# Kernel tuning notes

Measured on AMD Instinct MI355X. Metric: run time of the kernel, lower is better.

Reference implementation:

```python
import jax, jax.numpy as jnp
import numpy as np

E, B, DX, DC, DH, DO = 16, 4096, 128, 64, 1024, 128
DIN = DX + DC

def setup_inputs() -> dict:
    key = jax.random.key(0)
    ks = jax.random.split(key, 6)
    s1 = 1.0 / np.sqrt(DIN)
    s2 = 1.0 / np.sqrt(DH)
    return {
        "x": jax.random.normal(ks[0], (E, B, DX), dtype=jnp.float32),
        "cond": jax.random.normal(ks[1], (E, B, DC), dtype=jnp.float32),
        # stacked per-expert params, mirroring param_stacks ([E, ...])
        "W1": jax.random.uniform(ks[2], (E, DH, DIN), minval=-s1, maxval=s1, dtype=jnp.float32),
        "b1": jax.random.uniform(ks[3], (E, DH), minval=-s1, maxval=s1, dtype=jnp.float32),
        "W2": jax.random.uniform(ks[4], (E, DO, DH), minval=-s2, maxval=s2, dtype=jnp.float32),
        "b2": jax.random.uniform(ks[5], (E, DO), minval=-s2, maxval=s2, dtype=jnp.float32),
    }

def reference(x, cond, W1, b1, W2, b2):
    # vmap over experts == grouped GEMM with per-expert weight tiles
    xc = jnp.concatenate([x, cond], axis=-1)          # [E, B, DIN]
    h = jnp.einsum('ebi,ehi->ebh', xc, W1) + b1[:, None, :]  # [E, B, DH]
    h = jax.nn.relu(h)
    y = jnp.einsum('ebh,eoh->ebo', h, W2) + b2[:, None, :]   # [E, B, DO]
    return y
```

## Files before the change

### kernel.cpp

```cpp
#include <hip/hip_runtime.h>
#include <hip/hip_bf16.h>

#define E_   16
#define B_   4096
#define DX_  128
#define DC_  64
#define DIN_ 192
#define DH_  1024
#define DO_  128

#define BM 256
#define KC 64
#define NCHUNK 16
#define NT 1024

#define W1B_OFF 0
#define W1B_STR 12288
#define W2B_OFF 24576
#define W2B_STR 8192
#define HB_OFF  40960
#define HB_STR  16384

#define NW1U2 (E_ * DH_ * DIN_ / 4)
#define NW2U2 (E_ * DO_ * DH_ / 4)
#define WS_BYTES ((size_t)(NW1U2 + NW2U2) * 8)

typedef __attribute__((ext_vector_type(4))) float f32x4;
typedef __attribute__((ext_vector_type(8))) short bf16x8;

__device__ __forceinline__ unsigned f2bf_u(float f) {
    union { float f; unsigned u; } v; v.f = f;
    return (v.u + 0x7fffu + ((v.u >> 16) & 1u)) >> 16;
}
__device__ __forceinline__ uint2 pack4(float4 v) {
    uint2 r;
    r.x = f2bf_u(v.x) | (f2bf_u(v.y) << 16);
    r.y = f2bf_u(v.z) | (f2bf_u(v.w) << 16);
    return r;
}
__device__ __forceinline__ int swz(int r, int S, int cb) {
    return r * S + ((cb ^ ((r & 7) << 4)) >> 1);
}
__device__ __forceinline__ bf16x8 load8cvt(const float* p) {
    float4 a = *(const float4*)p;
    float4 b = *(const float4*)(p + 4);
    bf16x8 r;
    r[0] = (short)f2bf_u(a.x); r[1] = (short)f2bf_u(a.y);
    r[2] = (short)f2bf_u(a.z); r[3] = (short)f2bf_u(a.w);
    r[4] = (short)f2bf_u(b.x); r[5] = (short)f2bf_u(b.y);
    r[6] = (short)f2bf_u(b.z); r[7] = (short)f2bf_u(b.w);
    return r;
}
__device__ __forceinline__ void gld_lds16(const void* g, void* l) {
    __builtin_amdgcn_global_load_lds(
        (const __attribute__((address_space(1))) unsigned int*)g,
        (__attribute__((address_space(3))) unsigned int*)l, 16, 0, 0);
}

__global__ __launch_bounds__(256)
void convert_w(const float4* __restrict__ W1, const float4* __restrict__ W2,
               uint2* __restrict__ ws) {
    const int ntot = NW1U2 + NW2U2;
    for (int i = blockIdx.x * 256 + threadIdx.x; i < ntot; i += gridDim.x * 256) {
        if (i < NW1U2) {
            float4 v = W1[i];
            int e  = i / (DH_ * 48);
            int rr = i - e * (DH_ * 48);
            int hr = rr / 48, cu = rr - hr * 48;
            int ch = hr >> 6, r = hr & 63;
            int S  = swz(r, DIN_, cu * 8);
            ws[(size_t)(e * 16 + ch) * 3072 + (S >> 2)] = pack4(v);
        } else {
            ws[i] = pack4(W2[i - NW1U2]);
        }
    }
}

template <bool WS>
__global__ __launch_bounds__(NT, 4)
void moe_fused_kernel(const float* __restrict__ x, const float* __restrict__ cond,
                      const float* __restrict__ W1, const float* __restrict__ b1,
                      const float* __restrict__ W2, const float* __restrict__ b2,
                      const uint2* __restrict__ wsw, float* __restrict__ out) {
    __shared__ short LDSU[73728];

    const int bid = blockIdx.x;
    const int xcd = bid & 7;
    const int s   = bid >> 3;
    const int e   = 2 * xcd + (s & 1);
    const int row0 = (s >> 1) * BM;

    const int tid  = threadIdx.x;
    const int w    = tid >> 6;
    const int lane = tid & 63;
    const int lr   = lane & 15;
    const int lg   = lane >> 4;
    const int wo   = w & 1;
    const int wm   = w >> 1;

    const char*  ws1b = (const char*)wsw;
    const uint2* ws2  = wsw + NW1U2 + (size_t)e * (DO_ * DH_ / 4);
    const float4* g1f = (const float4*)(W1 + (size_t)e * DH_ * DIN_);
    const float*  g2f = W2 + (size_t)e * DO_ * DH_;

    bf16x8 xcreg[6];
    {
        const float* xrow = x    + (size_t)(e * B_ + row0 + w * 16 + lr) * DX_;
        const float* crow = cond + (size_t)(e * B_ + row0 + w * 16 + lr) * DC_;
#pragma unroll
        for (int kk = 0; kk < 4; ++kk) xcreg[kk] = load8cvt(xrow + kk * 32 + lg * 8);
#pragma unroll
        for (int kk = 4; kk < 6; ++kk) xcreg[kk] = load8cvt(crow + (kk - 4) * 32 + lg * 8);
    }

    uint2  r2[2]; float4 r2f[2]; float4 r1f[3];
    if constexpr (WS) {
        for (int q = w; q < 24; q += 16)
            gld_lds16(ws1b + (size_t)(e * 16 + 0) * 24576 + q * 1024 + lane * 16,
                      (char*)&LDSU[W1B_OFF] + q * 1024);
#pragma unroll
        for (int i = 0; i < 2; ++i) {
            int g = tid + NT * i, r = g >> 4, cc = g & 15;
            r2[i] = ws2[r * 256 + cc];
        }
    } else {
#pragma unroll
        for (int i = 0; i < 3; ++i) r1f[i] = g1f[tid + NT * i];
#pragma unroll
        for (int i = 0; i < 3; ++i) {
            int g = tid + NT * i, r = g / 48, cu = g - r * 48;
            *(uint2*)&LDSU[W1B_OFF + swz(r, DIN_, cu * 8)] = pack4(r1f[i]);
        }
#pragma unroll
        for (int i = 0; i < 3; ++i) r1f[i] = g1f[3072 + tid + NT * i];
#pragma unroll
        for (int i = 0; i < 2; ++i) {
            int g = tid + NT * i, r = g >> 4, cc = g & 15;
            r2f[i] = *(const float4*)(g2f + (size_t)r * DH_ + cc * 4);
        }
    }
    __syncthreads();

    f32x4 acc2[4][2] = {};

    for (int c = 0; c < NCHUNK; ++c) {
        const int pc = c & 1, pp = pc ^ 1;

#pragma unroll
        for (int i = 0; i < 2; ++i) {
            int g = tid + NT * i, r = g >> 4, cc = g & 15;
            uint2 pv; if constexpr (WS) pv = r2[i]; else pv = pack4(r2f[i]);
            *(uint2*)&LDSU[W2B_OFF + pc * W2B_STR + swz(r, KC, cc * 8)] = pv;
        }
        if (c + 1 < NCHUNK) {
            if constexpr (WS) {
                for (int q = w; q < 24; q += 16)
                    gld_lds16(ws1b + (size_t)(e * 16 + c + 1) * 24576 + q * 1024 + lane * 16,
                              (char*)&LDSU[W1B_OFF + pp * W1B_STR] + q * 1024);
            } else {
#pragma unroll
                for (int i = 0; i < 3; ++i) {
                    int g = tid + NT * i, r = g / 48, cu = g - r * 48;
                    *(uint2*)&LDSU[W1B_OFF + pp * W1B_STR + swz(r, DIN_, cu * 8)] = pack4(r1f[i]);
                }
                if (c + 2 < NCHUNK) {
#pragma unroll
                    for (int i = 0; i < 3; ++i) r1f[i] = g1f[(c + 2) * 3072 + tid + NT * i];
                }
            }
        }
        if (c + 1 < NCHUNK) {
            if constexpr (WS) {
#pragma unroll
                for (int i = 0; i < 2; ++i) {
                    int g = tid + NT * i, r = g >> 4, cc = g & 15;
                    r2[i] = ws2[r * 256 + (c + 1) * 16 + cc];
                }
            } else {
#pragma unroll
                for (int i = 0; i < 2; ++i) {
                    int g = tid + NT * i, r = g >> 4, cc = g & 15;
                    r2f[i] = *(const float4*)(g2f + (size_t)r * DH_ + (c + 1) * KC + cc * 4);
                }
            }
        }

        if (c > 0) {
#pragma unroll
            for (int kk = 0; kk < 2; ++kk) {
                bf16x8 aW2[4], bH[2];
#pragma unroll
                for (int of = 0; of < 4; ++of)
                    aW2[of] = *(const bf16x8*)&LDSU[W2B_OFF + pp * W2B_STR + swz(wo * 64 + of * 16 + lr, KC, kk * 64 + lg * 16)];
#pragma unroll
                for (int nf = 0; nf < 2; ++nf)
                    bH[nf] = *(const bf16x8*)&LDSU[HB_OFF + pp * HB_STR + swz(wm * 32 + nf * 16 + lr, KC, kk * 64 + lg * 16)];
#pragma unroll
                for (int of = 0; of < 4; ++of)
#pragma unroll
                    for (int nf = 0; nf < 2; ++nf)
                        acc2[of][nf] = __builtin_amdgcn_mfma_f32_16x16x32_bf16(aW2[of], bH[nf], acc2[of][nf], 0, 0, 0);
            }
        }

        f32x4 acc1[4] = {};
#pragma unroll
        for (int kk = 0; kk < 6; ++kk) {
            bf16x8 aW[4];
#pragma unroll
            for (int hf = 0; hf < 4; ++hf)
                aW[hf] = *(const bf16x8*)&LDSU[W1B_OFF + pc * W1B_STR + swz(hf * 16 + lr, DIN_, kk * 64 + lg * 16)];
#pragma unroll
            for (int hf = 0; hf < 4; ++hf)
                acc1[hf] = __builtin_amdgcn_mfma_f32_16x16x32_bf16(aW[hf], xcreg[kk], acc1[hf], 0, 0, 0);
        }
#pragma unroll
        for (int hf = 0; hf < 4; ++hf) {
            float4 b1f = *(const float4*)&b1[e * DH_ + c * KC + hf * 16 + lg * 4];
            float v0 = fmaxf(acc1[hf][0] + b1f.x, 0.f);
            float v1 = fmaxf(acc1[hf][1] + b1f.y, 0.f);
            float v2 = fmaxf(acc1[hf][2] + b1f.z, 0.f);
            float v3 = fmaxf(acc1[hf][3] + b1f.w, 0.f);
            uint2 hv;
            hv.x = f2bf_u(v0) | (f2bf_u(v1) << 16);
            hv.y = f2bf_u(v2) | (f2bf_u(v3) << 16);
            int m = w * 16 + lr;
            *(uint2*)&LDSU[HB_OFF + pc * HB_STR + swz(m, KC, hf * 32 + lg * 8)] = hv;
        }

        __syncthreads();
    }

#pragma unroll
    for (int kk = 0; kk < 2; ++kk) {
        bf16x8 aW2[4], bH[2];
#pragma unroll
        for (int of = 0; of < 4; ++of)
            aW2[of] = *(const bf16x8*)&LDSU[W2B_OFF + W2B_STR + swz(wo * 64 + of * 16 + lr, KC, kk * 64 + lg * 16)];
#pragma unroll
        for (int nf = 0; nf < 2; ++nf)
            bH[nf] = *(const bf16x8*)&LDSU[HB_OFF + HB_STR + swz(wm * 32 + nf * 16 + lr, KC, kk * 64 + lg * 16)];
#pragma unroll
        for (int of = 0; of < 4; ++of)
#pragma unroll
            for (int nf = 0; nf < 2; ++nf)
                acc2[of][nf] = __builtin_amdgcn_mfma_f32_16x16x32_bf16(aW2[of], bH[nf], acc2[of][nf], 0, 0, 0);
    }

#pragma unroll
    for (int of = 0; of < 4; ++of) {
        float4 b2f = *(const float4*)&b2[e * DO_ + wo * 64 + of * 16 + lg * 4];
#pragma unroll
        for (int nf = 0; nf < 2; ++nf) {
            int m = wm * 32 + nf * 16 + lr;
            float4 val;
            val.x = acc2[of][nf][0] + b2f.x;
            val.y = acc2[of][nf][1] + b2f.y;
            val.z = acc2[of][nf][2] + b2f.z;
            val.w = acc2[of][nf][3] + b2f.w;
            *(float4*)&out[(size_t)(e * B_ + row0 + m) * DO_ + wo * 64 + of * 16 + lg * 4] = val;
        }
    }
}

extern "C" void kernel_launch(void* const* d_in, const int* in_sizes, int n_in,
                              void* d_out, int out_size, void* d_ws, size_t ws_size,
                              hipStream_t stream) {
    const float* x    = (const float*)d_in[0];
    const float* cond = (const float*)d_in[1];
    const float* W1   = (const float*)d_in[2];
    const float* b1   = (const float*)d_in[3];
    const float* W2   = (const float*)d_in[4];
    const float* b2   = (const float*)d_in[5];
    float* out = (float*)d_out;

    dim3 grid(E_ * (B_ / BM));
    dim3 block(NT);

    const bool usews = (ws_size >= WS_BYTES) && (d_ws != nullptr);
    if (usews) {
        convert_w<<<2560, 256, 0, stream>>>((const float4*)W1, (const float4*)W2,
                                            (uint2*)d_ws);
        moe_fused_kernel<true><<<grid, block, 0, stream>>>(
            x, cond, W1, b1, W2, b2, (const uint2*)d_ws, out);
    } else {
        moe_fused_kernel<false><<<grid, block, 0, stream>>>(
            x, cond, W1, b1, W2, b2, (const uint2*)nullptr, out);
    }
}
```

Measured before the change: 155.3 us.

## Switch both GEMMs from 16x16x32 to 32x32x16 MFMA tiles

Replaces the 16x16x32 bf16 MFMA instructions with 32x32x16 ones in both layers, and remaps the waves to 32-row M bands with 32-wide hidden or output halves. The larger tiles use fewer LDS fragment loads per FLOP and fewer MFMA issues. In exchange, each wave now holds twice as many input-fragment registers (12 instead of 6) and accumulator layouts change. The LDS swizzle access patterns also change, which may introduce bank conflicts or register pressure at 4 waves per SIMD.

```diff
diff --git a/kernel.cpp b/kernel.cpp
--- a/kernel.cpp
+++ b/kernel.cpp
@@ -25,8 +25,9 @@
 #define NW2U2 (E_ * DO_ * DH_ / 4)
 #define WS_BYTES ((size_t)(NW1U2 + NW2U2) * 8)
 
-typedef __attribute__((ext_vector_type(4))) float f32x4;
-typedef __attribute__((ext_vector_type(8))) short bf16x8;
+typedef __attribute__((ext_vector_type(4)))  float f32x4;
+typedef __attribute__((ext_vector_type(16))) float f32x16;
+typedef __attribute__((ext_vector_type(8)))  short bf16x8;
 
 __device__ __forceinline__ unsigned f2bf_u(float f) {
     union { float f; unsigned u; } v; v.f = f;
@@ -93,24 +94,25 @@
     const int tid  = threadIdx.x;
     const int w    = tid >> 6;
     const int lane = tid & 63;
-    const int lr   = lane & 15;
-    const int lg   = lane >> 4;
-    const int wo   = w & 1;
-    const int wm   = w >> 1;
+    const int l31  = lane & 31;
+    const int lh   = lane >> 5;
+    const int mband = w >> 1;
+    const int hband = w & 1;
+    const int ohalf = w & 1;
 
     const char*  ws1b = (const char*)wsw;
     const uint2* ws2  = wsw + NW1U2 + (size_t)e * (DO_ * DH_ / 4);
     const float4* g1f = (const float4*)(W1 + (size_t)e * DH_ * DIN_);
     const float*  g2f = W2 + (size_t)e * DO_ * DH_;
 
-    bf16x8 xcreg[6];
+    bf16x8 xcreg[12];
     {
-        const float* xrow = x    + (size_t)(e * B_ + row0 + w * 16 + lr) * DX_;
-        const float* crow = cond + (size_t)(e * B_ + row0 + w * 16 + lr) * DC_;
-#pragma unroll
-        for (int kk = 0; kk < 4; ++kk) xcreg[kk] = load8cvt(xrow + kk * 32 + lg * 8);
-#pragma unroll
-        for (int kk = 4; kk < 6; ++kk) xcreg[kk] = load8cvt(crow + (kk - 4) * 32 + lg * 8);
+        const float* xrow = x    + (size_t)(e * B_ + row0 + mband * 32 + l31) * DX_;
+        const float* crow = cond + (size_t)(e * B_ + row0 + mband * 32 + l31) * DC_;
+#pragma unroll
+        for (int kb = 0; kb < 8; ++kb)  xcreg[kb] = load8cvt(xrow + kb * 16 + lh * 8);
+#pragma unroll
+        for (int kb = 8; kb < 12; ++kb) xcreg[kb] = load8cvt(crow + (kb - 8) * 16 + lh * 8);
     }
 
     uint2  r2[2]; float4 r2f[2]; float4 r1f[3];
@@ -141,7 +143,7 @@
     }
     __syncthreads();
 
-    f32x4 acc2[4][2] = {};
+    f32x16 acc2[2] = {};
 
     for (int c = 0; c < NCHUNK; ++c) {
         const int pc = c & 1, pp = pc ^ 1;
@@ -187,79 +189,72 @@
 
         if (c > 0) {
 #pragma unroll
-            for (int kk = 0; kk < 2; ++kk) {
-                bf16x8 aW2[4], bH[2];
-#pragma unroll
-                for (int of = 0; of < 4; ++of)
-                    aW2[of] = *(const bf16x8*)&LDSU[W2B_OFF + pp * W2B_STR + swz(wo * 64 + of * 16 + lr, KC, kk * 64 + lg * 16)];
-#pragma unroll
-                for (int nf = 0; nf < 2; ++nf)
-                    bH[nf] = *(const bf16x8*)&LDSU[HB_OFF + pp * HB_STR + swz(wm * 32 + nf * 16 + lr, KC, kk * 64 + lg * 16)];
-#pragma unroll
-                for (int of = 0; of < 4; ++of)
-#pragma unroll
-                    for (int nf = 0; nf < 2; ++nf)
-                        acc2[of][nf] = __builtin_amdgcn_mfma_f32_16x16x32_bf16(aW2[of], bH[nf], acc2[of][nf], 0, 0, 0);
-            }
-        }
-
-        f32x4 acc1[4] = {};
-#pragma unroll
-        for (int kk = 0; kk < 6; ++kk) {
-            bf16x8 aW[4];
-#pragma unroll
-            for (int hf = 0; hf < 4; ++hf)
-                aW[hf] = *(const bf16x8*)&LDSU[W1B_OFF + pc * W1B_STR + swz(hf * 16 + lr, DIN_, kk * 64 + lg * 16)];
-#pragma unroll
-            for (int hf = 0; hf < 4; ++hf)
-                acc1[hf] = __builtin_amdgcn_mfma_f32_16x16x32_bf16(aW[hf], xcreg[kk], acc1[hf], 0, 0, 0);
-        }
-#pragma unroll
-        for (int hf = 0; hf < 4; ++hf) {
-            float4 b1f = *(const float4*)&b1[e * DH_ + c * KC + hf * 16 + lg * 4];
-            float v0 = fmaxf(acc1[hf][0] + b1f.x, 0.f);
-            float v1 = fmaxf(acc1[hf][1] + b1f.y, 0.f);
-            float v2 = fmaxf(acc1[hf][2] + b1f.z, 0.f);
-            float v3 = fmaxf(acc1[hf][3] + b1f.w, 0.f);
-            uint2 hv;
-            hv.x = f2bf_u(v0) | (f2bf_u(v1) << 16);
-            hv.y = f2bf_u(v2) | (f2bf_u(v3) << 16);
-            int m = w * 16 + lr;
-            *(uint2*)&LDSU[HB_OFF + pc * HB_STR + swz(m, KC, hf * 32 + lg * 8)] = hv;
+            for (int kb = 0; kb < 4; ++kb) {
+                bf16x8 bH = *(const bf16x8*)&LDSU[HB_OFF + pp * HB_STR +
+                                swz(mband * 32 + l31, KC, kb * 32 + lh * 16)];
+#pragma unroll
+                for (int ot = 0; ot < 2; ++ot) {
+                    bf16x8 aW2 = *(const bf16x8*)&LDSU[W2B_OFF + pp * W2B_STR +
+                                    swz(ohalf * 64 + ot * 32 + l31, KC, kb * 32 + lh * 16)];
+                    acc2[ot] = __builtin_amdgcn_mfma_f32_32x32x16_bf16(aW2, bH, acc2[ot], 0, 0, 0);
+                }
+            }
+        }
+
+        f32x16 acc1 = {};
+#pragma unroll
+        for (int kb = 0; kb < 12; ++kb) {
+            bf16x8 aW = *(const bf16x8*)&LDSU[W1B_OFF + pc * W1B_STR +
+                            swz(hband * 32 + l31, DIN_, kb * 32 + lh * 16)];
+            acc1 = __builtin_amdgcn_mfma_f32_32x32x16_bf16(aW, xcreg[kb], acc1, 0, 0, 0);
+        }
+        {
+            int m = mband * 32 + l31;
+#pragma unroll
+            for (int rg = 0; rg < 4; ++rg) {
+                float4 b1f = *(const float4*)&b1[e * DH_ + c * KC + hband * 32 + rg * 8 + lh * 4];
+                float v0 = fmaxf(acc1[rg * 4 + 0] + b1f.x, 0.f);
+                float v1 = fmaxf(acc1[rg * 4 + 1] + b1f.y, 0.f);
+                float v2 = fmaxf(acc1[rg * 4 + 2] + b1f.z, 0.f);
+                float v3 = fmaxf(acc1[rg * 4 + 3] + b1f.w, 0.f);
+                uint2 hv;
+                hv.x = f2bf_u(v0) | (f2bf_u(v1) << 16);
+                hv.y = f2bf_u(v2) | (f2bf_u(v3) << 16);
+                *(uint2*)&LDSU[HB_OFF + pc * HB_STR +
+                               swz(m, KC, hband * 64 + rg * 16 + lh * 8)] = hv;
+            }
         }
 
         __syncthreads();
     }
 
 #pragma unroll
-    for (int kk = 0; kk < 2; ++kk) {
-        bf16x8 aW2[4], bH[2];
-#pragma unroll
-        for (int of = 0; of < 4; ++of)
-            aW2[of] = *(const bf16x8*)&LDSU[W2B_OFF + W2B_STR + swz(wo * 64 + of * 16 + lr, KC, kk * 64 + lg * 16)];
-#pragma unroll
-        for (int nf = 0; nf < 2; ++nf)
-            bH[nf] = *(const bf16x8*)&LDSU[HB_OFF + HB_STR + swz(wm * 32 + nf * 16 + lr, KC, kk * 64 + lg * 16)];
-#pragma unroll
-        for (int of = 0; of < 4; ++of)
-#pragma unroll
-            for (int nf = 0; nf < 2; ++nf)
-                acc2[of][nf] = __builtin_amdgcn_mfma_f32_16x16x32_bf16(aW2[of], bH[nf], acc2[of][nf], 0, 0, 0);
-    }
-
-#pragma unroll
-    for (int of = 0; of < 4; ++of) {
-        float4 b2f = *(const float4*)&b2[e * DO_ + wo * 64 + of * 16 + lg * 4];
-#pragma unroll
-        for (int nf = 0; nf < 2; ++nf) {
-            int m = wm * 32 + nf * 16 + lr;
-            float4 val;
-            val.x = acc2[of][nf][0] + b2f.x;
-            val.y = acc2[of][nf][1] + b2f.y;
-            val.z = acc2[of][nf][2] + b2f.z;
-            val.w = acc2[of][nf][3] + b2f.w;
-            *(float4*)&out[(size_t)(e * B_ + row0 + m) * DO_ + wo * 64 + of * 16 + lg * 4] = val;
-        }
+    for (int kb = 0; kb < 4; ++kb) {
+        bf16x8 bH = *(const bf16x8*)&LDSU[HB_OFF + HB_STR +
+                        swz(mband * 32 + l31, KC, kb * 32 + lh * 16)];
+#pragma unroll
+        for (int ot = 0; ot < 2; ++ot) {
+            bf16x8 aW2 = *(const bf16x8*)&LDSU[W2B_OFF + W2B_STR +
+                            swz(ohalf * 64 + ot * 32 + l31, KC, kb * 32 + lh * 16)];
+            acc2[ot] = __builtin_amdgcn_mfma_f32_32x32x16_bf16(aW2, bH, acc2[ot], 0, 0, 0);
+        }
+    }
+
+    {
+        int m = mband * 32 + l31;
+#pragma unroll
+        for (int ot = 0; ot < 2; ++ot)
+#pragma unroll
+            for (int rg = 0; rg < 4; ++rg) {
+                int ob = ohalf * 64 + ot * 32 + rg * 8 + lh * 4;
+                float4 b2f = *(const float4*)&b2[e * DO_ + ob];
+                float4 val;
+                val.x = acc2[ot][rg * 4 + 0] + b2f.x;
+                val.y = acc2[ot][rg * 4 + 1] + b2f.y;
+                val.z = acc2[ot][rg * 4 + 2] + b2f.z;
+                val.w = acc2[ot][rg * 4 + 3] + b2f.w;
+                *(float4*)&out[(size_t)(e * B_ + row0 + m) * DO_ + ob] = val;
+            }
     }
 }
 
```

Result: slower. 189.0 us (+21.7%).
